# Performance work log

Measured on AMD Instinct MI355X. Metric: run time of the kernel, lower is better.

## Reference

```python
import jax, jax.numpy as jnp
import numpy as np

BATCH, N_FEAT, N_CH = 16384, 16, 1
EXP_ORDER, OUT_DIM = 3, 256


def expansion_indices(n, exp_order):
    """Replicates the original nested-loop index bookkeeping statically.

    Returns a list of (J, P) per expansion pass: the new block of monomials is
    x[:, J, :] * epd[:, P, :]. All indices in a pass reference terms produced in
    earlier passes, so one concat per pass is exactly equivalent to the original.
    """
    Id = np.arange(n)
    M = n
    steps = []
    for _ in range(exp_order):
        Js, Ps = [], []
        for j in range(n):
            rng = np.arange(Id[j], Id[n - 1] + 1)
            Js.append(np.full(rng.shape, j))
            Ps.append(rng)
            Id[j] = M
            M += rng.size
        steps.append((np.concatenate(Js), np.concatenate(Ps)))
    return steps, M

STEPS, M_TOTAL = expansion_indices(N_FEAT, EXP_ORDER)  # M_TOTAL == 4844


def taylor_expand(x):
    # x: [B, n, Q] -> epd: [B, M_TOTAL, Q] (all monomials of degree 1..EXP_ORDER+1)
    epd = x
    for J, P in STEPS:
        new = x[:, J, :] * epd[:, P, :]
        epd = jnp.concatenate([epd, new], axis=1)
    return epd


def setup_inputs() -> dict:
    key = jax.random.key(0)
    k1, k2, k3 = jax.random.split(key, 3)
    inputs = jax.random.normal(k1, (BATCH, N_FEAT, N_CH), dtype=jnp.float32)
    # 'dl' weight init: uniform(-1/sqrt(shape[0]), 1/sqrt(shape[0]))
    w_scale = 1.0 / np.sqrt(OUT_DIM)
    W = jax.random.uniform(k2, (OUT_DIM, M_TOTAL), minval=-w_scale, maxval=w_scale, dtype=jnp.float32)
    # 'uniform' bias init: uniform(-0.2, 0.2), shape [out, 1]
    b = jax.random.uniform(k3, (OUT_DIM, 1), minval=-0.2, maxval=0.2, dtype=jnp.float32)
    return {"inputs": inputs, "W": W, "b": b}


def reference(inputs, W, b):
    # cp_type='tanh': first cp block applies tanh, second block is identity for tanh
    x = jnp.tanh(inputs)
    epd = taylor_expand(x)                         # [B, M_TOTAL, Q]
    out = jnp.einsum('rm,bmq->brq', W, epd) + b    # [B, OUT_DIM, Q]
    return jax.nn.relu(out)                        # act_type='relu'
```

## Files before the change

kernel.cpp:

```cpp
#include <hip/hip_runtime.h>

#define BATCH   16384
#define NF      16
#define OUTD    256
#define MTOT    4844
#define NK      5120
#define NCHUNK  80
#define NIV     20
#define TROW    155
#define NCREAL  5080

struct Plan {
    unsigned cplan[NCHUNK * 16];
    short    perm[NK];
    unsigned d2t[136];
    int ncols; int nreal; bool ok;
};

constexpr Plan make_plan() {
    Plan P{};
    int posx[17] = {};
    for (int c = 0; c <= 16; ++c) posx[c] = 17 * c - c * (c - 1) / 2;
    int S1t[16], Id2t[16], b3[16], b4[16];
    for (int j = 0; j < 16; ++j) { S1t[j] = 16 * j - j * (j - 1) / 2; Id2t[j] = 16 + S1t[j]; }
    { int s = 152; for (int j = 0; j < 16; ++j) { b3[j] = s; s += 152 - Id2t[j]; } }
    { int s = 968; for (int j = 0; j < 16; ++j) { b4[j] = s; s += 968 - b3[j]; } }
    { int idx = 0;
      for (int c = 0; c < 16; ++c)
        for (int d = c; d < 16; ++d)
            P.d2t[idx++] = (unsigned)posx[c] | ((unsigned)posx[d] << 10)
                         | ((unsigned)(posx[c] + 1 + (d - c)) << 20);
    }
    for (int q = 0; q < NCHUNK * 16; ++q) P.cplan[q] = 153u | (152u << 16);
    for (int k = 0; k < NK; ++k) P.perm[k] = -1;

    int k = 0;
    for (int p = 0; p < 152; ++p) {
        if ((k & 3) == 0) P.cplan[k >> 2] = 152u | ((unsigned)p << 16);
        int c = 0; while (posx[c + 1] <= p) ++c;
        int m;
        if (p == posx[c]) m = c;
        else { int d = c + (p - posx[c] - 1); m = 16 + S1t[c] + (d - c); }
        P.perm[k++] = (short)m;
    }
    for (int b = 0; b < 16; ++b)
      for (int a = 0; a <= b; ++a) {
        const int L = posx[a] + 1 + (b - a);
        const int st = posx[b], len = 152 - st, plen = (len + 3) & ~3;
        for (int off = 0; off < plen; ++off) {
            if ((k & 3) == 0) P.cplan[k >> 2] = (unsigned)L | ((unsigned)(st + off) << 16);
            if (off < len) {
                const int p = st + off;
                int c = 0; while (posx[c + 1] <= p) ++c;
                int m;
                if (p == posx[c]) {
                    m = b3[a] + (16 + S1t[b] + (c - b)) - Id2t[a];
                } else {
                    const int d = c + (p - posx[c] - 1);
                    const int o3 = b3[b] + (16 + S1t[c] + (d - c)) - Id2t[b];
                    m = b4[a] + o3 - b3[a];
                }
                P.perm[k] = (short)m;
            }
            ++k;
        }
      }
    P.ncols = k;
    unsigned bm[152] = {};
    int cnt = 0; bool ok = (k == NCREAL);
    for (int kk = 0; kk < NK; ++kk) {
        const int m = P.perm[kk];
        if (m >= 0) {
            if (m >= MTOT || (bm[m >> 5] & (1u << (m & 31)))) { ok = false; break; }
            bm[m >> 5] |= 1u << (m & 31); ++cnt;
        }
    }
    if (cnt != MTOT) ok = false;
    P.nreal = cnt; P.ok = ok;
    return P;
}
constexpr Plan h_plan = make_plan();
static_assert(h_plan.ncols == NCREAL, "padded col count");
static_assert(h_plan.ok, "perm bijection onto [0,4844)");
__device__ const Plan g_plan = make_plan();

typedef __attribute__((ext_vector_type(8))) short    bf16x8;
typedef __attribute__((ext_vector_type(4))) float    f32x4;
typedef __attribute__((ext_vector_type(4))) unsigned uint4v;

__device__ inline unsigned bfpack2(float lo, float hi) {
    unsigned ul = __float_as_uint(lo), uh = __float_as_uint(hi);
    ul = (ul + 0x7fffu + ((ul >> 16) & 1u)) >> 16;
    uh = (uh + 0x7fffu + ((uh >> 16) & 1u)) & 0xffff0000u;
    return ul | uh;
}

__global__ __launch_bounds__(256) void wconv_kernel(
    const float* __restrict__ W, unsigned* __restrict__ Wb)
{
    const int r = blockIdx.x;
    const float* Wr = W + (size_t)r * MTOT;
    for (int i = threadIdx.x; i < NK / 2; i += 256) {
        const int m0 = g_plan.perm[2 * i], m1 = g_plan.perm[2 * i + 1];
        const float f0 = (m0 >= 0) ? Wr[m0] : 0.f;
        const float f1 = (m1 >= 0) ? Wr[m1] : 0.f;
        Wb[(size_t)r * (NK / 2) + i] = bfpack2(f0, f1);
    }
}

#define T_BYTES   (64 * TROW * 4)
#define AS_BYTES  (8 * 8 * 64 * 8 * 2)
#define LDS_BYTES (T_BYTES + AS_BYTES)

__global__ __launch_bounds__(512, 2) void fused_kernel(
    const float* __restrict__ x,
    const unsigned short* __restrict__ Wb,
    const float* __restrict__ bias,
    float* __restrict__ C)
{
    extern __shared__ char smem[];
    float* T = (float*)smem;
    unsigned short* As = (unsigned short*)(smem + T_BYTES);

    const int t = threadIdx.x, l = t & 63, wid = t >> 6;
    const size_t m0 = (size_t)blockIdx.x * 64;

    uint4v ePA[4], ePB[4];
    auto loadPlan = [&](int iv, uint4v (&e)[4]) {
#pragma unroll
        for (int cc = 0; cc < 4; ++cc)
            e[cc] = *(const uint4v*)(g_plan.cplan + (iv * 4 + cc) * 16 + wid * 4);
    };
    const int w = wid - 4, lr = l & 15, lk = l >> 4;
    const unsigned short* wbase = Wb + (size_t)(w * 64 + lr) * NK + lk * 8;
    bf16x8 bA[4][2], bB[4][2];
    auto prefB = [&](int c, bf16x8 (&bf)[4][2]) {
#pragma unroll
        for (int ni = 0; ni < 4; ++ni)
#pragma unroll
            for (int ks = 0; ks < 2; ++ks)
                bf[ni][ks] = *(const bf16x8*)(wbase + (size_t)ni * 16 * NK
                                              + (size_t)c * 64 + ks * 32);
    };
    if (wid < 4) loadPlan(0, ePA); else prefB(0, bA);

#pragma unroll
    for (int i = 0; i < 2; ++i) {
        const int v = t * 2 + i;
        const int r = v >> 4, f = v & 15;
        const int pf = 17 * f - f * (f - 1) / 2;
        T[r * TROW + pf] = tanhf(x[(m0 + r) * NF + f]);
    }
    if (t < 64) { T[t*TROW + 152] = 1.f; T[t*TROW + 153] = 0.f; T[t*TROW + 154] = 0.f; }
    __syncthreads();
    {
        const int r = t >> 3, s = t & 7, base = r * TROW;
#pragma unroll
        for (int i = 0; i < 17; ++i) {
            const unsigned e = g_plan.d2t[s + 8 * i];
            T[base + (e >> 20)] = T[base + (e & 1023u)] * T[base + ((e >> 10) & 1023u)];
        }
    }
    __syncthreads();

    const int pb = l * TROW;
    auto expand = [&](int c, const uint4v& e) {
        float v[16];
#pragma unroll
        for (int q = 0; q < 4; ++q) {
            const unsigned eq = e[q];
            const float lv = T[pb + (eq & 0xffffu)];
            const int   r0 = pb + (int)(eq >> 16);
#pragma unroll
            for (int u = 0; u < 4; ++u) v[q * 4 + u] = lv * T[r0 + u];
        }
        uint4v o0, o1;
        o0[0]=bfpack2(v[0],v[1]);   o0[1]=bfpack2(v[2],v[3]);
        o0[2]=bfpack2(v[4],v[5]);   o0[3]=bfpack2(v[6],v[7]);
        o1[0]=bfpack2(v[8],v[9]);   o1[1]=bfpack2(v[10],v[11]);
        o1[2]=bfpack2(v[12],v[13]); o1[3]=bfpack2(v[14],v[15]);
        const int slot = c & 7;
        *(uint4v*)&As[(((slot * 8 + 2 * wid    ) * 64) + l) * 8] = o0;
        *(uint4v*)&As[(((slot * 8 + 2 * wid + 1) * 64) + l) * 8] = o1;
    };

    f32x4 acc[4][4];
#pragma unroll
    for (int i = 0; i < 4; ++i)
#pragma unroll
        for (int j = 0; j < 4; ++j) acc[i][j] = (f32x4){0.f, 0.f, 0.f, 0.f};

    auto domfma = [&](int c, bf16x8 (&bf)[4][2]) {
        const int slot = c & 7;
        bf16x8 af[4][2];
#pragma unroll
        for (int mi = 0; mi < 4; ++mi)
#pragma unroll
            for (int ks = 0; ks < 2; ++ks)
                af[mi][ks] = *(const bf16x8*)
                    &As[(((slot * 8 + ks * 4 + lk) * 64) + mi * 16 + lr) * 8];
#pragma unroll
        for (int ks = 0; ks < 2; ++ks)
#pragma unroll
            for (int mi = 0; mi < 4; ++mi)
#pragma unroll
                for (int ni = 0; ni < 4; ++ni)
                    acc[mi][ni] = __builtin_amdgcn_mfma_f32_16x16x32_bf16(
                        af[mi][ks], bf[ni][ks], acc[mi][ni], 0, 0, 0);
    };

    auto pbody = [&](int i, uint4v (&eUse)[4], uint4v (&eLoad)[4]) {
        if (i + 1 < NIV) {
#pragma unroll
            for (int cc = 0; cc < 4; ++cc) expand((i + 1) * 4 + cc, eUse[cc]);
        }
        if (i + 2 < NIV) loadPlan(i + 2, eLoad);
    };
    auto cbody = [&](int i) {
#pragma unroll
        for (int cc = 0; cc < 4; ++cc) {
            const int c = i * 4 + cc;
            const int nc = (c + 1 < NCHUNK) ? c + 1 : c;
            if (cc & 1) { prefB(nc, bA); domfma(c, bB); }
            else        { prefB(nc, bB); domfma(c, bA); }
        }
    };

    if (wid < 4) {
#pragma unroll
        for (int cc = 0; cc < 4; ++cc) expand(cc, ePA[cc]);
        loadPlan(1, ePB);
    }
    __syncthreads();

    for (int i2 = 0; i2 < NIV; i2 += 2) {
        if (wid < 4) pbody(i2, ePB, ePA); else cbody(i2);
        __syncthreads();
        if (wid < 4) pbody(i2 + 1, ePA, ePB); else cbody(i2 + 1);
        __syncthreads();
    }

    if (wid >= 4) {
#pragma unroll
        for (int ni = 0; ni < 4; ++ni) {
            const int col = w * 64 + ni * 16 + lr;
            const float bv = bias[col];
#pragma unroll
            for (int mi = 0; mi < 4; ++mi) {
                const size_t r0 = m0 + mi * 16 + lk * 4;
#pragma unroll
                for (int j = 0; j < 4; ++j)
                    C[(r0 + j) * OUTD + col] = fmaxf(acc[mi][ni][j] + bv, 0.f);
            }
        }
    }
}

extern "C" void kernel_launch(void* const* d_in, const int* in_sizes, int n_in,
                              void* d_out, int out_size, void* d_ws, size_t ws_size,
                              hipStream_t stream)
{
    const float* x    = (const float*)d_in[0];
    const float* W    = (const float*)d_in[1];
    const float* bias = (const float*)d_in[2];
    float* out        = (float*)d_out;

    unsigned* Wb = (unsigned*)d_ws;
    (void)hipFuncSetAttribute((const void*)fused_kernel,
                              hipFuncAttributeMaxDynamicSharedMemorySize, LDS_BYTES);
    wconv_kernel<<<OUTD, 256, 0, stream>>>(W, Wb);
    fused_kernel<<<BATCH / 64, 512, LDS_BYTES, stream>>>(
        x, (const unsigned short*)Wb, bias, out);
}
```

Before: 151.7 us.

## Drop producer/consumer warp specialization; all waves expand and run MFMA

Previously four waves generated bf16 monomial chunks into LDS while four other waves ran MFMAs. Now all eight waves do both: each expands half as many entries per chunk and computes a 64x32 output slice with half the B fragments and accumulators. The goal is to remove the imbalance where one wave group idles while the other works, and to lower register pressure per wave. In exchange, every wave reads the full A tile from LDS, so total LDS A-fragment traffic doubles, and expand and MFMA now share each wave's issue slots.

```diff
diff --git a/kernel.cpp b/kernel.cpp
--- a/kernel.cpp
+++ b/kernel.cpp
@@ -87,6 +87,7 @@
 typedef __attribute__((ext_vector_type(8))) short    bf16x8;
 typedef __attribute__((ext_vector_type(4))) float    f32x4;
 typedef __attribute__((ext_vector_type(4))) unsigned uint4v;
+typedef __attribute__((ext_vector_type(2))) unsigned u32x2;
 
 __device__ inline unsigned bfpack2(float lo, float hi) {
     unsigned ul = __float_as_uint(lo), uh = __float_as_uint(hi);
@@ -123,26 +124,27 @@
     unsigned short* As = (unsigned short*)(smem + T_BYTES);
 
     const int t = threadIdx.x, l = t & 63, wid = t >> 6;
+    const int lr = l & 15, lk = l >> 4;
     const size_t m0 = (size_t)blockIdx.x * 64;
 
-    uint4v ePA[4], ePB[4];
-    auto loadPlan = [&](int iv, uint4v (&e)[4]) {
+    u32x2 ePA[4], ePB[4];
+    auto loadPlan = [&](int iv, u32x2 (&e)[4]) {
 #pragma unroll
         for (int cc = 0; cc < 4; ++cc)
-            e[cc] = *(const uint4v*)(g_plan.cplan + (iv * 4 + cc) * 16 + wid * 4);
-    };
-    const int w = wid - 4, lr = l & 15, lk = l >> 4;
-    const unsigned short* wbase = Wb + (size_t)(w * 64 + lr) * NK + lk * 8;
-    bf16x8 bA[4][2], bB[4][2];
-    auto prefB = [&](int c, bf16x8 (&bf)[4][2]) {
-#pragma unroll
-        for (int ni = 0; ni < 4; ++ni)
+            e[cc] = *(const u32x2*)(g_plan.cplan + (iv * 4 + cc) * 16 + 2 * wid);
+    };
+    const unsigned short* wbase = Wb + (size_t)(wid * 32 + lr) * NK + lk * 8;
+    bf16x8 bA[2][2], bB[2][2];
+    auto prefB = [&](int c, bf16x8 (&bf)[2][2]) {
+#pragma unroll
+        for (int ni = 0; ni < 2; ++ni)
 #pragma unroll
             for (int ks = 0; ks < 2; ++ks)
                 bf[ni][ks] = *(const bf16x8*)(wbase + (size_t)ni * 16 * NK
                                               + (size_t)c * 64 + ks * 32);
     };
-    if (wid < 4) loadPlan(0, ePA); else prefB(0, bA);
+    loadPlan(0, ePA);
+    prefB(0, bA);
 
 #pragma unroll
     for (int i = 0; i < 2; ++i) {
@@ -164,33 +166,30 @@
     __syncthreads();
 
     const int pb = l * TROW;
-    auto expand = [&](int c, const uint4v& e) {
-        float v[16];
-#pragma unroll
-        for (int q = 0; q < 4; ++q) {
-            const unsigned eq = e[q];
+    auto expand = [&](int c, const u32x2& e2) {
+        float v[8];
+#pragma unroll
+        for (int q = 0; q < 2; ++q) {
+            const unsigned eq = e2[q];
             const float lv = T[pb + (eq & 0xffffu)];
             const int   r0 = pb + (int)(eq >> 16);
 #pragma unroll
             for (int u = 0; u < 4; ++u) v[q * 4 + u] = lv * T[r0 + u];
         }
-        uint4v o0, o1;
-        o0[0]=bfpack2(v[0],v[1]);   o0[1]=bfpack2(v[2],v[3]);
-        o0[2]=bfpack2(v[4],v[5]);   o0[3]=bfpack2(v[6],v[7]);
-        o1[0]=bfpack2(v[8],v[9]);   o1[1]=bfpack2(v[10],v[11]);
-        o1[2]=bfpack2(v[12],v[13]); o1[3]=bfpack2(v[14],v[15]);
+        uint4v o;
+        o[0] = bfpack2(v[0], v[1]); o[1] = bfpack2(v[2], v[3]);
+        o[2] = bfpack2(v[4], v[5]); o[3] = bfpack2(v[6], v[7]);
         const int slot = c & 7;
-        *(uint4v*)&As[(((slot * 8 + 2 * wid    ) * 64) + l) * 8] = o0;
-        *(uint4v*)&As[(((slot * 8 + 2 * wid + 1) * 64) + l) * 8] = o1;
-    };
-
-    f32x4 acc[4][4];
+        *(uint4v*)&As[(((slot * 8 + wid) * 64) + l) * 8] = o;
+    };
+
+    f32x4 acc[4][2];
 #pragma unroll
     for (int i = 0; i < 4; ++i)
 #pragma unroll
-        for (int j = 0; j < 4; ++j) acc[i][j] = (f32x4){0.f, 0.f, 0.f, 0.f};
-
-    auto domfma = [&](int c, bf16x8 (&bf)[4][2]) {
+        for (int j = 0; j < 2; ++j) acc[i][j] = (f32x4){0.f, 0.f, 0.f, 0.f};
+
+    auto mfmaChunk = [&](int c, bf16x8 (&bf)[2][2]) {
         const int slot = c & 7;
         bf16x8 af[4][2];
 #pragma unroll
@@ -204,54 +203,45 @@
 #pragma unroll
             for (int mi = 0; mi < 4; ++mi)
 #pragma unroll
-                for (int ni = 0; ni < 4; ++ni)
+                for (int ni = 0; ni < 2; ++ni)
                     acc[mi][ni] = __builtin_amdgcn_mfma_f32_16x16x32_bf16(
                         af[mi][ks], bf[ni][ks], acc[mi][ni], 0, 0, 0);
     };
 
-    auto pbody = [&](int i, uint4v (&eUse)[4], uint4v (&eLoad)[4]) {
-        if (i + 1 < NIV) {
-#pragma unroll
-            for (int cc = 0; cc < 4; ++cc) expand((i + 1) * 4 + cc, eUse[cc]);
-        }
-        if (i + 2 < NIV) loadPlan(i + 2, eLoad);
-    };
-    auto cbody = [&](int i) {
+    auto body = [&](int iv, u32x2 (&eUse)[4], u32x2 (&eLoad)[4]) {
 #pragma unroll
         for (int cc = 0; cc < 4; ++cc) {
-            const int c = i * 4 + cc;
+            const int c  = iv * 4 + cc;
             const int nc = (c + 1 < NCHUNK) ? c + 1 : c;
-            if (cc & 1) { prefB(nc, bA); domfma(c, bB); }
-            else        { prefB(nc, bB); domfma(c, bA); }
-        }
-    };
-
-    if (wid < 4) {
-#pragma unroll
-        for (int cc = 0; cc < 4; ++cc) expand(cc, ePA[cc]);
-        loadPlan(1, ePB);
-    }
+            if (cc & 1) { prefB(nc, bA); mfmaChunk(c, bB); }
+            else        { prefB(nc, bB); mfmaChunk(c, bA); }
+            if (iv + 1 < NIV) expand((iv + 1) * 4 + cc, eUse[cc]);
+        }
+        if (iv + 2 < NIV) loadPlan(iv + 2, eLoad);
+    };
+
+#pragma unroll
+    for (int cc = 0; cc < 4; ++cc) expand(cc, ePA[cc]);
+    loadPlan(1, ePB);
     __syncthreads();
 
     for (int i2 = 0; i2 < NIV; i2 += 2) {
-        if (wid < 4) pbody(i2, ePB, ePA); else cbody(i2);
+        body(i2, ePB, ePA);
         __syncthreads();
-        if (wid < 4) pbody(i2 + 1, ePA, ePB); else cbody(i2 + 1);
+        body(i2 + 1, ePA, ePB);
         __syncthreads();
     }
 
-    if (wid >= 4) {
-#pragma unroll
-        for (int ni = 0; ni < 4; ++ni) {
-            const int col = w * 64 + ni * 16 + lr;
-            const float bv = bias[col];
-#pragma unroll
-            for (int mi = 0; mi < 4; ++mi) {
-                const size_t r0 = m0 + mi * 16 + lk * 4;
-#pragma unroll
-                for (int j = 0; j < 4; ++j)
-                    C[(r0 + j) * OUTD + col] = fmaxf(acc[mi][ni][j] + bv, 0.f);
-            }
+#pragma unroll
+    for (int ni = 0; ni < 2; ++ni) {
+        const int col = wid * 32 + ni * 16 + lr;
+        const float bv = bias[col];
+#pragma unroll
+        for (int mi = 0; mi < 4; ++mi) {
+            const size_t r0 = m0 + mi * 16 + lk * 4;
+#pragma unroll
+            for (int j = 0; j < 4; ++j)
+                C[(r0 + j) * OUTD + col] = fmaxf(acc[mi][ni][j] + bv, 0.f);
         }
     }
 }
```

Result: slower. 155.9 us (+2.7%).
